# Performance work log

Measured on AMD Instinct MI355X. Metric: run time of the kernel, lower is better.

The kernel has to match this reference:

```python
import jax, jax.numpy as jnp
import numpy as np

B, N, D = 128, 256, 384  # pairs, nodes per graph (n1 == n2), embedding dim


def setup_inputs() -> dict:
    key = jax.random.key(0)
    k1, k2 = jax.random.split(key)
    x1 = jax.random.normal(k1, (B, N, D), dtype=jnp.float32)
    x2 = jax.random.normal(k2, (B, N, D), dtype=jnp.float32)
    return {"x1": x1, "x2": x2}


def _match_one(a, b):
    """Greedy max-weight bipartite matching score for one pair (n1 == n2 == N).
    Faithful to MNEMatch: submat = a @ b^T, then min(n1,n2) iterations of
    global argmax + row/col removal; sum of picked entries / max(n1,n2), tanh.
    Row/col removal is expressed as masking on the full matrix so shapes stay
    static (equivalent math to TF's gather-based shrink when n1 == n2)."""
    n = a.shape[0]
    S = a @ b.T  # [N, N] score matrix
    neg = jnp.finfo(S.dtype).min

    def step(carry, _):
        rmask, cmask = carry  # bool [N] each: rows/cols still alive
        alive = rmask[:, None] & cmask[None, :]
        idx = jnp.argmax(jnp.where(alive, S, neg))  # flat argmax over live entries
        r = idx // n
        c = idx % n
        val = S[r, c]
        return (rmask.at[r].set(False), cmask.at[c].set(False)), val

    init = (jnp.ones(n, dtype=bool), jnp.ones(n, dtype=bool))
    _, vals = jax.lax.scan(step, init, None, length=n)  # match_num = N picks
    # total_num = max(n1, n2) = N; inneract = tanh; output shape [1]
    return jnp.reshape(jnp.tanh(jnp.sum(vals) / n), (1,))


def reference(x1, x2):
    # _call over a list of pairs -> tf.stack => [B, 1]
    return jax.vmap(_match_one)(x1, x2)
```

## Files before the change

### kernel.cpp

```cpp
#include <hip/hip_runtime.h>
#include <cmath>

#define NN 256
#define DD 384
#define CAPS 2048
#define THRESH 40.0f
#define KCAP 64
#define RSTRIDE 257
#define KK2 4096

typedef unsigned long long ull;
typedef short bf16x8 __attribute__((ext_vector_type(8)));
typedef float f32x4  __attribute__((ext_vector_type(4)));

__device__ __forceinline__ unsigned bfpack2(float lo, float hi) {
  return (__float_as_uint(hi) & 0xFFFF0000u) | (__float_as_uint(lo) >> 16);
}

__global__ __launch_bounds__(256) void gemm_bt_mfma(const float* __restrict__ X1,
                                                    const float* __restrict__ X2,
                                                    float* __restrict__ S) {
  const int pair  = blockIdx.z;
  const int rbase = blockIdx.y * 128;
  const int cbase = blockIdx.x * 64;

  __shared__ unsigned short As[128][40];
  __shared__ unsigned short Bs[64][40];

  const int tid   = threadIdx.x;
  const int lane  = tid & 63;
  const int wave  = tid >> 6;
  const int q     = lane >> 4, mi = lane & 15;

  const int srowA = tid >> 1, halfA = tid & 1;
  const int srowB = tid >> 2, qB    = tid & 3;

  const float* Abase = X1 + (size_t)pair * NN * DD + (size_t)(rbase + srowA) * DD + halfA * 16;
  const float* Bbase = X2 + (size_t)pair * NN * DD + (size_t)(cbase + srowB) * DD + qB * 8;

  f32x4 acc[2][4] = {};

  float4 pa0, pa1, pa2, pa3, pb0, pb1;
  {
    const float4* ap = (const float4*)(Abase);
    const float4* bp = (const float4*)(Bbase);
    pa0 = ap[0]; pa1 = ap[1]; pa2 = ap[2]; pa3 = ap[3];
    pb0 = bp[0]; pb1 = bp[1];
  }

  for (int k0 = 0; k0 < DD; k0 += 32) {
    __syncthreads();
    {
      uint4 w0 = make_uint4(bfpack2(pa0.x,pa0.y), bfpack2(pa0.z,pa0.w),
                            bfpack2(pa1.x,pa1.y), bfpack2(pa1.z,pa1.w));
      uint4 w1 = make_uint4(bfpack2(pa2.x,pa2.y), bfpack2(pa2.z,pa2.w),
                            bfpack2(pa3.x,pa3.y), bfpack2(pa3.z,pa3.w));
      *(uint4*)&As[srowA][halfA*16]     = w0;
      *(uint4*)&As[srowA][halfA*16 + 8] = w1;
      uint4 v0 = make_uint4(bfpack2(pb0.x,pb0.y), bfpack2(pb0.z,pb0.w),
                            bfpack2(pb1.x,pb1.y), bfpack2(pb1.z,pb1.w));
      *(uint4*)&Bs[srowB][qB*8] = v0;
    }
    __syncthreads();
    const int kn = k0 + 32;
    if (kn < DD) {
      const float4* ap = (const float4*)(Abase + kn);
      const float4* bp = (const float4*)(Bbase + kn);
      pa0 = ap[0]; pa1 = ap[1]; pa2 = ap[2]; pa3 = ap[3];
      pb0 = bp[0]; pb1 = bp[1];
    }
    bf16x8 af[2], bf[4];
#pragma unroll
    for (int i = 0; i < 2; ++i) af[i] = *(const bf16x8*)&As[wave*32 + i*16 + mi][q*8];
#pragma unroll
    for (int j = 0; j < 4; ++j) bf[j] = *(const bf16x8*)&Bs[j*16 + mi][q*8];
#pragma unroll
    for (int i = 0; i < 2; ++i)
#pragma unroll
      for (int j = 0; j < 4; ++j)
        acc[i][j] = __builtin_amdgcn_mfma_f32_16x16x32_bf16(af[i], bf[j], acc[i][j], 0, 0, 0);
  }

  float* Sp = S + (size_t)pair * NN * NN;
#pragma unroll
  for (int i = 0; i < 2; ++i)
#pragma unroll
    for (int j = 0; j < 4; ++j)
#pragma unroll
      for (int r2 = 0; r2 < 4; ++r2) {
        const int rowg = rbase + wave*32 + i*16 + q*4 + r2;
        const int colg = cbase + j*16 + mi;
        Sp[(size_t)rowg * NN + colg] = acc[i][j][r2];
      }
}

#define DPP_STEP(ctrl, rmask)                                                  \
  {                                                                            \
    int vi  = __float_as_int(v);                                               \
    int v2b = __builtin_amdgcn_update_dpp(vi, vi, (ctrl), (rmask), 0xf, false);\
    int i2  = __builtin_amdgcn_update_dpp(c,  c,  (ctrl), (rmask), 0xf, false);\
    float v2 = __int_as_float(v2b);                                            \
    if (v2 > v || (v2 == v && i2 < c)) { v = v2; c = i2; }                     \
  }

__device__ __forceinline__ void dpp_argmax(float& v, int& c) {
  DPP_STEP(0x111, 0xf)
  DPP_STEP(0x112, 0xf)
  DPP_STEP(0x114, 0xf)
  DPP_STEP(0x118, 0xf)
  DPP_STEP(0x142, 0xa)
  DPP_STEP(0x143, 0xc)
}
#undef DPP_STEP

__device__ __forceinline__ float rdlane_f(float v, int l) {
  return __int_as_float(__builtin_amdgcn_readlane(__float_as_int(v), l));
}

__device__ __forceinline__ int nth_set4(ull m0, ull m1, ull m2, ull m3, int n) {
  int base = 0; ull m = m0;
  int c = __popcll(m);
  if (n >= c) { n -= c; m = m1; base = 64; c = __popcll(m);
    if (n >= c) { n -= c; m = m2; base = 128; c = __popcll(m);
      if (n >= c) { n -= c; m = m3; base = 192; } } }
  for (int i = 0; i < n; ++i) m &= m - 1;
  return m ? (base + (int)__builtin_ctzll(m)) : 0;
}

__device__ __forceinline__ void scan_own_row(const float* __restrict__ rowp,
                                             ull a0, ull a1, ull a2, ull a3,
                                             float& mv, int& ac) {
  float v = -INFINITY; int c = 0;
#pragma unroll
  for (int g = 0; g < 4; ++g) {
    const ull am = (g==0) ? a0 : (g==1) ? a1 : (g==2) ? a2 : a3;
#pragma unroll 8
    for (int j = 0; j < 64; ++j) {
      if ((am >> j) & 1ull) {
        const float x = rowp[g*64 + j];
        if (x > v) { v = x; c = g*64 + j; }
      }
    }
  }
  mv = v; ac = c;
}

__global__ __launch_bounds__(1024) void match_pair(const float* __restrict__ S,
                                                   float* __restrict__ out) {
  const int pair = blockIdx.x;
  const float* Sp = S + (size_t)pair * NN * NN;
  const int tid  = threadIdx.x;
  const int lane = tid & 63;
  const int wv   = tid >> 6;

  __shared__ ull keys2[KK2];
  __shared__ float rows[KCAP * RSTRIDE];
  __shared__ int lcount;
  __shared__ ull sh_mask[8];
  __shared__ float sh_sum;
  __shared__ int sh_picks;

  if (tid == 0) lcount = 0;
  __syncthreads();

  const float4* S4 = (const float4*)Sp;
#pragma unroll 4
  for (int i4 = tid; i4 < NN*NN/4; i4 += 1024) {
    float4 x = S4[i4];
    float xv[4] = {x.x, x.y, x.z, x.w};
#pragma unroll
    for (int e = 0; e < 4; ++e) {
      if (xv[e] > THRESH) {
        unsigned b = __float_as_uint(xv[e]);
        unsigned u = (b & 0x80000000u) ? ~b : (b | 0x80000000u);
        int pos = atomicAdd(&lcount, 1);
        if (pos < CAPS)
          keys2[pos] = ((ull)(~u) << 32) | (unsigned)(i4*4 + e);
      }
    }
  }
  __syncthreads();
  int count = lcount;
  if (count > CAPS) count = 0;
  for (int i = count + tid; i < CAPS; i += 1024) keys2[i] = ~0ull;
  __syncthreads();

  for (unsigned kk = 2; kk <= CAPS; kk <<= 1)
    for (unsigned j = kk >> 1; j > 0; j >>= 1) {
      for (unsigned i = tid; i < CAPS; i += 1024) {
        unsigned ixj = i ^ j;
        if (ixj > i) {
          ull a = keys2[i], b = keys2[ixj];
          bool asc = ((i & kk) == 0);
          if ((a > b) == asc) { keys2[i] = b; keys2[ixj] = a; }
        }
      }
      __syncthreads();
    }

  if (wv == 0) {
    unsigned rowAlive = 0xFu, colAlive = 0xFu;
    float sum = 0.0f;
    int picks = 0;
    for (int base = 0; base < count && picks < NN; base += 64) {
      const ull key = keys2[base + lane];
      const int flat = (int)(unsigned)key;
      const int r = (flat >> 8) & 255, c = flat & 255;
      const unsigned u = ~(unsigned)(key >> 32);
      const float val = __uint_as_float((u & 0x80000000u) ? (u ^ 0x80000000u) : ~u);
      const bool valid = (base + lane) < count;

      const int rbits = __builtin_amdgcn_ds_bpermute((r & 63) << 2, (int)rowAlive);
      const int cbits = __builtin_amdgcn_ds_bpermute((c & 63) << 2, (int)colAlive);
      bool alive = valid && (((rbits >> (r >> 6)) & 1) != 0) && (((cbits >> (c >> 6)) & 1) != 0);

      while (true) {
        const ull mb = __ballot(alive);
        if (!mb) break;
        const int t   = __builtin_ctzll(mb);
        const int r_t = __builtin_amdgcn_readlane(r, t);
        const int c_t = __builtin_amdgcn_readlane(c, t);
        sum += rdlane_f(val, t);
        ++picks;
        alive = alive && (r != r_t) && (c != c_t);
        rowAlive &= ~((lane == (r_t & 63) ? 1u : 0u) << (r_t >> 6));
        colAlive &= ~((lane == (c_t & 63) ? 1u : 0u) << (c_t >> 6));
        if (picks == NN) break;
      }
    }
    ull m[8];
#pragma unroll
    for (int i = 0; i < 4; ++i) m[i]     = __ballot(((rowAlive >> i) & 1u) != 0);
#pragma unroll
    for (int i = 0; i < 4; ++i) m[4 + i] = __ballot(((colAlive >> i) & 1u) != 0);
    if (lane == 0) {
#pragma unroll
      for (int i = 0; i < 8; ++i) sh_mask[i] = m[i];
      sh_sum   = sum;
      sh_picks = picks;
    }
  }
  __syncthreads();

  const ull arow0 = sh_mask[0], arow1 = sh_mask[1], arow2 = sh_mask[2], arow3 = sh_mask[3];
  const ull acol0 = sh_mask[4], acol1 = sh_mask[5], acol2 = sh_mask[6], acol3 = sh_mask[7];
  float sum = sh_sum;
  const int picks = sh_picks;

  if (picks >= NN) {
    if (tid == 0) out[pair] = tanhf(sum / (float)NN);
    return;
  }
  const int k = NN - picks;

  if (k > KCAP) {
    if (wv != 0) return;
    ull bc0 = acol0, bc1 = acol1, bc2 = acol2, bc3 = acol3;
    float rm[4]; int ra[4];
#pragma unroll
    for (int i = 0; i < 4; ++i) { rm[i] = -INFINITY; ra[i] = -1; }
    {
      if ((arow0 >> lane) & 1ull) scan_own_row(Sp + (size_t)lane * NN, bc0, bc1, bc2, bc3, rm[0], ra[0]);
      if ((arow1 >> lane) & 1ull) scan_own_row(Sp + (size_t)(64 + lane) * NN, bc0, bc1, bc2, bc3, rm[1], ra[1]);
      if ((arow2 >> lane) & 1ull) scan_own_row(Sp + (size_t)(128 + lane) * NN, bc0, bc1, bc2, bc3, rm[2], ra[2]);
      if ((arow3 >> lane) & 1ull) scan_own_row(Sp + (size_t)(192 + lane) * NN, bc0, bc1, bc2, bc3, rm[3], ra[3]);
    }
    for (int it = picks; it < NN; ++it) {
      float v = rm[0]; int c = lane;
      if (rm[1] > v) { v = rm[1]; c = 64 + lane; }
      if (rm[2] > v) { v = rm[2]; c = 128 + lane; }
      if (rm[3] > v) { v = rm[3]; c = 192 + lane; }
      dpp_argmax(v, c);
      const int br = __builtin_amdgcn_readlane(c, 63);
      sum += rdlane_f(v, 63);

      const int bslot = br >> 6, blane = br & 63;
      int myra = ra[0];
      if (bslot == 1) myra = ra[1];
      if (bslot == 2) myra = ra[2];
      if (bslot == 3) myra = ra[3];
      const int bc = __builtin_amdgcn_readlane(myra, blane);

      if (lane == blane) {
        if (bslot == 0) { rm[0] = -INFINITY; ra[0] = -1; }
        if (bslot == 1) { rm[1] = -INFINITY; ra[1] = -1; }
        if (bslot == 2) { rm[2] = -INFINITY; ra[2] = -1; }
        if (bslot == 3) { rm[3] = -INFINITY; ra[3] = -1; }
      }
      { const ull cb = ~(1ull << (bc & 63));
        if      (bc < 64)  bc0 &= cb;
        else if (bc < 128) bc1 &= cb;
        else if (bc < 192) bc2 &= cb;
        else               bc3 &= cb; }

#pragma unroll
      for (int i = 0; i < 4; ++i) {
        const bool st = (ra[i] == bc);
        if (__ballot(st)) {
          if (st) {
            float nv; int nc;
            scan_own_row(Sp + (size_t)(i*64 + lane) * NN, bc0, bc1, bc2, bc3, nv, nc);
            rm[i] = nv; ra[i] = nc;
          }
        }
      }
    }
    if (lane == 0) out[pair] = tanhf(sum / (float)NN);
    return;
  }

  const int slot = tid >> 4;
  const int seg  = tid & 15;
  if (slot < k) {
    const int r = nth_set4(arow0, arow1, arow2, arow3, slot);
    const float4* src = (const float4*)(Sp + (size_t)r * NN + seg * 16);
    float* dst = &rows[slot * RSTRIDE + seg * 16];
#pragma unroll
    for (int i = 0; i < 4; ++i) {
      float4 v = src[i];
      dst[i*4 + 0] = v.x; dst[i*4 + 1] = v.y;
      dst[i*4 + 2] = v.z; dst[i*4 + 3] = v.w;
    }
    const int w  = seg >> 2;
    const int sb = (seg & 3) * 16;
    const ull aw = (w==0) ? acol0 : (w==1) ? acol1 : (w==2) ? acol2 : acol3;
    int crank = 0;
    if (w > 0) crank += __popcll(acol0);
    if (w > 1) crank += __popcll(acol1);
    if (w > 2) crank += __popcll(acol2);
    crank += __popcll(aw & ((1ull << sb) - 1ull));
    const float* rp = &rows[slot * RSTRIDE + w * 64];
    for (int j = sb; j < sb + 16; ++j) {
      if ((aw >> j) & 1ull) {
        const unsigned b = __float_as_uint(rp[j]);
        const unsigned u = (b & 0x80000000u) ? ~b : (b | 0x80000000u);
        keys2[slot * k + crank] = ((ull)(~u) << 32) | (unsigned)((slot << 6) | crank);
        ++crank;
      }
    }
  }
  const int nkk = k * k;
  int n2 = 64; while (n2 < nkk) n2 <<= 1;
  for (int i = nkk + tid; i < n2; i += 1024) keys2[i] = ~0ull;
  __syncthreads();

  for (unsigned kk = 2; kk <= (unsigned)n2; kk <<= 1)
    for (unsigned j = kk >> 1; j > 0; j >>= 1) {
      for (unsigned i = tid; i < (unsigned)n2; i += 1024) {
        unsigned ixj = i ^ j;
        if (ixj > i) {
          ull a = keys2[i], b = keys2[ixj];
          bool asc = ((i & kk) == 0);
          if ((a > b) == asc) { keys2[i] = b; keys2[ixj] = a; }
        }
      }
      __syncthreads();
    }
  if (wv != 0) return;

  ull rAlive = (k == 64) ? ~0ull : ((1ull << k) - 1ull);
  ull cAlive = rAlive;
  int tpicks = 0;
  for (int base = 0; base < nkk && tpicks < k; base += 64) {
    const ull key = keys2[base + lane];
    const int rc = (int)(unsigned)key & 0xFFF;
    const int rs = (rc >> 6) & 63, cs = rc & 63;
    const unsigned u = ~(unsigned)(key >> 32);
    const float val = __uint_as_float((u & 0x80000000u) ? (u ^ 0x80000000u) : ~u);
    const bool valid = (base + lane) < nkk;

    bool alive = valid && (((rAlive >> rs) & 1ull) != 0) && (((cAlive >> cs) & 1ull) != 0);
    while (true) {
      const ull mb = __ballot(alive);
      if (!mb) break;
      const int t    = __builtin_ctzll(mb);
      const int rs_t = __builtin_amdgcn_readlane(rs, t);
      const int cs_t = __builtin_amdgcn_readlane(cs, t);
      sum += rdlane_f(val, t);
      ++tpicks;
      alive = alive && (rs != rs_t) && (cs != cs_t);
      rAlive &= ~(1ull << rs_t);
      cAlive &= ~(1ull << cs_t);
      if (tpicks == k) break;
    }
  }

  if (lane == 0) out[pair] = tanhf(sum / (float)NN);
}

extern "C" void kernel_launch(void* const* d_in, const int* in_sizes, int n_in,
                              void* d_out, int out_size, void* d_ws, size_t ws_size,
                              hipStream_t stream) {
  const float* x1 = (const float*)d_in[0];
  const float* x2 = (const float*)d_in[1];
  float* out = (float*)d_out;
  float* S   = (float*)d_ws;

  const int B = in_sizes[0] / (NN * DD);

  dim3 ggrid(NN / 64, NN / 128, B);
  gemm_bt_mfma<<<ggrid, 256, 0, stream>>>(x1, x2, S);
  match_pair<<<B, 1024, 0, stream>>>(S, out);
}
```

Baseline: 270.9 us.

## Fuse bf16 MFMA GEMM into matching kernel and use wave-local bitonic stages

Removes the separate GEMM kernel and computes the per-pair 256x256 score matrix inside the matching block, in two 128-column passes. LDS is reused for the A and B tiles. Threshold candidates are collected directly from the accumulators, so the full S matrix no longer has to be re-read from global memory. The bitonic sort is also restructured so that sub-stages fitting inside a wave-owned chunk use wave barriers instead of block-wide __syncthreads. In exchange, the GEMM now runs with only B blocks of 1024 threads, which may leave the GEMM phase with lower parallelism than the separate 3D-grid launch had.

```diff
diff --git a/kernel.cpp b/kernel.cpp
--- a/kernel.cpp
+++ b/kernel.cpp
@@ -15,83 +15,6 @@
 
 __device__ __forceinline__ unsigned bfpack2(float lo, float hi) {
   return (__float_as_uint(hi) & 0xFFFF0000u) | (__float_as_uint(lo) >> 16);
-}
-
-__global__ __launch_bounds__(256) void gemm_bt_mfma(const float* __restrict__ X1,
-                                                    const float* __restrict__ X2,
-                                                    float* __restrict__ S) {
-  const int pair  = blockIdx.z;
-  const int rbase = blockIdx.y * 128;
-  const int cbase = blockIdx.x * 64;
-
-  __shared__ unsigned short As[128][40];
-  __shared__ unsigned short Bs[64][40];
-
-  const int tid   = threadIdx.x;
-  const int lane  = tid & 63;
-  const int wave  = tid >> 6;
-  const int q     = lane >> 4, mi = lane & 15;
-
-  const int srowA = tid >> 1, halfA = tid & 1;
-  const int srowB = tid >> 2, qB    = tid & 3;
-
-  const float* Abase = X1 + (size_t)pair * NN * DD + (size_t)(rbase + srowA) * DD + halfA * 16;
-  const float* Bbase = X2 + (size_t)pair * NN * DD + (size_t)(cbase + srowB) * DD + qB * 8;
-
-  f32x4 acc[2][4] = {};
-
-  float4 pa0, pa1, pa2, pa3, pb0, pb1;
-  {
-    const float4* ap = (const float4*)(Abase);
-    const float4* bp = (const float4*)(Bbase);
-    pa0 = ap[0]; pa1 = ap[1]; pa2 = ap[2]; pa3 = ap[3];
-    pb0 = bp[0]; pb1 = bp[1];
-  }
-
-  for (int k0 = 0; k0 < DD; k0 += 32) {
-    __syncthreads();
-    {
-      uint4 w0 = make_uint4(bfpack2(pa0.x,pa0.y), bfpack2(pa0.z,pa0.w),
-                            bfpack2(pa1.x,pa1.y), bfpack2(pa1.z,pa1.w));
-      uint4 w1 = make_uint4(bfpack2(pa2.x,pa2.y), bfpack2(pa2.z,pa2.w),
-                            bfpack2(pa3.x,pa3.y), bfpack2(pa3.z,pa3.w));
-      *(uint4*)&As[srowA][halfA*16]     = w0;
-      *(uint4*)&As[srowA][halfA*16 + 8] = w1;
-      uint4 v0 = make_uint4(bfpack2(pb0.x,pb0.y), bfpack2(pb0.z,pb0.w),
-                            bfpack2(pb1.x,pb1.y), bfpack2(pb1.z,pb1.w));
-      *(uint4*)&Bs[srowB][qB*8] = v0;
-    }
-    __syncthreads();
-    const int kn = k0 + 32;
-    if (kn < DD) {
-      const float4* ap = (const float4*)(Abase + kn);
-      const float4* bp = (const float4*)(Bbase + kn);
-      pa0 = ap[0]; pa1 = ap[1]; pa2 = ap[2]; pa3 = ap[3];
-      pb0 = bp[0]; pb1 = bp[1];
-    }
-    bf16x8 af[2], bf[4];
-#pragma unroll
-    for (int i = 0; i < 2; ++i) af[i] = *(const bf16x8*)&As[wave*32 + i*16 + mi][q*8];
-#pragma unroll
-    for (int j = 0; j < 4; ++j) bf[j] = *(const bf16x8*)&Bs[j*16 + mi][q*8];
-#pragma unroll
-    for (int i = 0; i < 2; ++i)
-#pragma unroll
-      for (int j = 0; j < 4; ++j)
-        acc[i][j] = __builtin_amdgcn_mfma_f32_16x16x32_bf16(af[i], bf[j], acc[i][j], 0, 0, 0);
-  }
-
-  float* Sp = S + (size_t)pair * NN * NN;
-#pragma unroll
-  for (int i = 0; i < 2; ++i)
-#pragma unroll
-    for (int j = 0; j < 4; ++j)
-#pragma unroll
-      for (int r2 = 0; r2 < 4; ++r2) {
-        const int rowg = rbase + wave*32 + i*16 + q*4 + r2;
-        const int colg = cbase + j*16 + mi;
-        Sp[(size_t)rowg * NN + colg] = acc[i][j][r2];
-      }
 }
 
 #define DPP_STEP(ctrl, rmask)                                                  \
@@ -145,58 +68,133 @@
   mv = v; ac = c;
 }
 
-__global__ __launch_bounds__(1024) void match_pair(const float* __restrict__ S,
+__device__ __forceinline__ void bitonic_lds(ull* __restrict__ keys, int n,
+                                            int tid, int lane, int wv) {
+  const int chunk = ((n >> 4) < 64) ? 64 : (n >> 4);
+  const int wbase = wv * chunk;
+
+#define CMPSW(I, KK)                                                           \
+  {                                                                            \
+    int ixj = (I) ^ j;                                                         \
+    if (ixj > (I)) {                                                           \
+      ull a = keys[(I)], b = keys[ixj];                                        \
+      bool asc = (((I) & (KK)) == 0);                                          \
+      if ((a > b) == asc) { keys[(I)] = b; keys[ixj] = a; }                    \
+    }                                                                          \
+  }
+
+  if (wbase < n) {
+    for (int kk = 2; kk <= chunk; kk <<= 1)
+      for (int j = kk >> 1; j > 0; j >>= 1) {
+        for (int t = lane; t < chunk; t += 64) { int i = wbase + t; CMPSW(i, kk) }
+        __builtin_amdgcn_wave_barrier();
+      }
+  }
+  __syncthreads();
+  for (int kk = chunk << 1; kk <= n; kk <<= 1) {
+    for (int j = kk >> 1; j >= chunk; j >>= 1) {
+      for (int i = tid; i < n; i += 1024) CMPSW(i, kk)
+      __syncthreads();
+    }
+    if (wbase < n) {
+      for (int j = chunk >> 1; j > 0; j >>= 1) {
+        for (int t = lane; t < chunk; t += 64) { int i = wbase + t; CMPSW(i, kk) }
+        __builtin_amdgcn_wave_barrier();
+      }
+    }
+    __syncthreads();
+  }
+#undef CMPSW
+}
+
+__global__ __launch_bounds__(1024) void match_pair(const float* __restrict__ X1,
+                                                   const float* __restrict__ X2,
+                                                   float* __restrict__ S,
                                                    float* __restrict__ out) {
   const int pair = blockIdx.x;
-  const float* Sp = S + (size_t)pair * NN * NN;
   const int tid  = threadIdx.x;
   const int lane = tid & 63;
   const int wv   = tid >> 6;
 
+  __shared__ float rows[KCAP * RSTRIDE];
   __shared__ ull keys2[KK2];
-  __shared__ float rows[KCAP * RSTRIDE];
   __shared__ int lcount;
   __shared__ ull sh_mask[8];
   __shared__ float sh_sum;
   __shared__ int sh_picks;
 
+  const float* X1p = X1 + (size_t)pair * NN * DD;
+  const float* X2p = X2 + (size_t)pair * NN * DD;
+  float* Sp = S + (size_t)pair * NN * NN;
+
   if (tid == 0) lcount = 0;
-  __syncthreads();
-
-  const float4* S4 = (const float4*)Sp;
-#pragma unroll 4
-  for (int i4 = tid; i4 < NN*NN/4; i4 += 1024) {
-    float4 x = S4[i4];
-    float xv[4] = {x.x, x.y, x.z, x.w};
-#pragma unroll
-    for (int e = 0; e < 4; ++e) {
-      if (xv[e] > THRESH) {
-        unsigned b = __float_as_uint(xv[e]);
-        unsigned u = (b & 0x80000000u) ? ~b : (b | 0x80000000u);
-        int pos = atomicAdd(&lcount, 1);
-        if (pos < CAPS)
-          keys2[pos] = ((ull)(~u) << 32) | (unsigned)(i4*4 + e);
-      }
-    }
-  }
-  __syncthreads();
+
+  {
+    unsigned short (*As)[40] = (unsigned short(*)[40])rows;
+    unsigned short (*Bs)[40] = (unsigned short(*)[40])(rows + 5120);
+    const int q  = lane >> 4, mi = lane & 15;
+    const int srA = tid >> 2, qkA = tid & 3;
+    const int srB = tid >> 3, qkB = tid & 7;
+    const float* aptr = X1p + (size_t)srA * DD + qkA * 8;
+
+    for (int pass = 0; pass < 2; ++pass) {
+      const int colbase = pass * 128;
+      const float* bptr = X2p + (size_t)(colbase + srB) * DD + qkB * 4;
+
+      f32x4 acc[8] = {};
+      float4 pa0 = *(const float4*)(aptr);
+      float4 pa1 = *(const float4*)(aptr + 4);
+      float4 pb0 = *(const float4*)(bptr);
+
+      for (int k0 = 0; k0 < DD; k0 += 32) {
+        __syncthreads();
+        {
+          uint4 wA = make_uint4(bfpack2(pa0.x,pa0.y), bfpack2(pa0.z,pa0.w),
+                                bfpack2(pa1.x,pa1.y), bfpack2(pa1.z,pa1.w));
+          *(uint4*)&As[srA][qkA*8] = wA;
+          uint2 wB = make_uint2(bfpack2(pb0.x,pb0.y), bfpack2(pb0.z,pb0.w));
+          *(uint2*)&Bs[srB][qkB*4] = wB;
+        }
+        __syncthreads();
+        const int kn = k0 + 32;
+        if (kn < DD) {
+          pa0 = *(const float4*)(aptr + kn);
+          pa1 = *(const float4*)(aptr + kn + 4);
+          pb0 = *(const float4*)(bptr + kn);
+        }
+        bf16x8 af = *(const bf16x8*)&As[wv*16 + mi][q*8];
+#pragma unroll
+        for (int t = 0; t < 8; ++t) {
+          bf16x8 bf = *(const bf16x8*)&Bs[t*16 + mi][q*8];
+          acc[t] = __builtin_amdgcn_mfma_f32_16x16x32_bf16(af, bf, acc[t], 0, 0, 0);
+        }
+      }
+#pragma unroll
+      for (int t = 0; t < 8; ++t)
+#pragma unroll
+        for (int r = 0; r < 4; ++r) {
+          const int rowg = wv*16 + q*4 + r;
+          const int colg = colbase + t*16 + mi;
+          const float v = acc[t][r];
+          Sp[(size_t)rowg * NN + colg] = v;
+          if (v > THRESH) {
+            unsigned b = __float_as_uint(v);
+            unsigned u = (b & 0x80000000u) ? ~b : (b | 0x80000000u);
+            int pos = atomicAdd(&lcount, 1);
+            if (pos < CAPS)
+              keys2[pos] = ((ull)(~u) << 32) | (unsigned)(rowg * NN + colg);
+          }
+        }
+      __syncthreads();
+    }
+  }
+
   int count = lcount;
   if (count > CAPS) count = 0;
   for (int i = count + tid; i < CAPS; i += 1024) keys2[i] = ~0ull;
   __syncthreads();
 
-  for (unsigned kk = 2; kk <= CAPS; kk <<= 1)
-    for (unsigned j = kk >> 1; j > 0; j >>= 1) {
-      for (unsigned i = tid; i < CAPS; i += 1024) {
-        unsigned ixj = i ^ j;
-        if (ixj > i) {
-          ull a = keys2[i], b = keys2[ixj];
-          bool asc = ((i & kk) == 0);
-          if ((a > b) == asc) { keys2[i] = b; keys2[ixj] = a; }
-        }
-      }
-      __syncthreads();
-    }
+  bitonic_lds(keys2, CAPS, tid, lane, wv);
 
   if (wv == 0) {
     unsigned rowAlive = 0xFu, colAlive = 0xFu;
@@ -344,18 +342,8 @@
   for (int i = nkk + tid; i < n2; i += 1024) keys2[i] = ~0ull;
   __syncthreads();
 
-  for (unsigned kk = 2; kk <= (unsigned)n2; kk <<= 1)
-    for (unsigned j = kk >> 1; j > 0; j >>= 1) {
-      for (unsigned i = tid; i < (unsigned)n2; i += 1024) {
-        unsigned ixj = i ^ j;
-        if (ixj > i) {
-          ull a = keys2[i], b = keys2[ixj];
-          bool asc = ((i & kk) == 0);
-          if ((a > b) == asc) { keys2[i] = b; keys2[ixj] = a; }
-        }
-      }
-      __syncthreads();
-    }
+  bitonic_lds(keys2, n2, tid, lane, wv);
+
   if (wv != 0) return;
 
   ull rAlive = (k == 64) ? ~0ull : ((1ull << k) - 1ull);
@@ -398,7 +386,5 @@
 
   const int B = in_sizes[0] / (NN * DD);
 
-  dim3 ggrid(NN / 64, NN / 128, B);
-  gemm_bt_mfma<<<ggrid, 256, 0, stream>>>(x1, x2, S);
-  match_pair<<<B, 1024, 0, stream>>>(S, out);
-}
+  match_pair<<<B, 1024, 0, stream>>>(x1, x2, S, out);
+}
```

After: 253.2 us. 6.5% less time.
